# Kernel tuning notes

Measured on AMD Instinct MI355X. Metric: run time of the kernel, lower is better.

The kernel has to match this reference:

```python
import jax, jax.numpy as jnp
import numpy as np


def setup_inputs() -> dict:
    key = jax.random.key(0)
    k0, k1, k2, k3, k4 = jax.random.split(key, 5)
    B, N, H, d, kproj = 4, 2048, 8, 32, 256
    queries = jax.random.normal(k0, (B, N, H, d), dtype=jnp.float32)
    keys = jax.random.normal(k1, (B, N, H, d), dtype=jnp.float32)
    values = jax.random.normal(k2, (B, N, H, d), dtype=jnp.float32)
    # Linformer sequence projections [N, k]; scaled so projected K/V keep unit-ish variance
    E_proj = jax.random.normal(k3, (N, kproj), dtype=jnp.float32) * 0.02
    F_proj = jax.random.normal(k4, (N, kproj), dtype=jnp.float32) * 0.02
    return {"queries": queries, "keys": keys, "values": values,
            "E_proj": E_proj, "F_proj": F_proj}


def reference(queries, keys, values, E_proj, F_proj):
    """Hybrid attention of dsfa_former:
      (1) FullAttention with triangular causal mask (manual einsum+softmax)
      (2) LinearAttentionHead: Linformer-style sequence projection of K/V via E/F.
    Dropout is identity (eval). Returns (out_full, out_lin), each [B, N, H, d].
    """
    B, N, H, d = queries.shape
    scale = 1.0 / jnp.sqrt(jnp.asarray(d, queries.dtype))

    # ---- FullAttention (causal) ----
    scores = jnp.einsum('blhe,bshe->bhls', queries, keys)  # [B,H,N,N]
    causal = jnp.triu(jnp.ones((N, N), dtype=bool), k=1)   # True above diag -> masked
    scores = jnp.where(causal, -jnp.inf, scores)
    A = jax.nn.softmax(scale * scores, axis=-1)
    out_full = jnp.einsum('bhls,bshd->blhd', A, values)    # [B,N,H,d]

    # ---- LinearAttentionHead (Linformer, no causal mask since kp != N) ----
    Qb = queries.transpose(0, 2, 1, 3)  # [B,H,N,d]
    Kb = keys.transpose(0, 2, 1, 3)
    Vb = values.transpose(0, 2, 1, 3)
    Kp = jnp.einsum('bhnd,nk->bhkd', Kb, E_proj)           # [B,H,k,d]
    Vp = jnp.einsum('bhnd,nk->bhkd', Vb, F_proj)           # [B,H,k,d]
    s_lin = jnp.einsum('bhnd,bhkd->bhnk', Qb, Kp) * scale  # d_k == d
    P = jax.nn.softmax(s_lin, axis=-1)
    out_lin = jnp.einsum('bhnk,bhkd->bhnd', P, Vp).transpose(0, 2, 1, 3)  # [B,N,H,d]

    return out_full, out_lin
```

## Files before the change

### kernel.cpp

```cpp
#include <hip/hip_runtime.h>
#include <hip/hip_bf16.h>


typedef __bf16 bf16x8 __attribute__((ext_vector_type(8)));
typedef float f32x4 __attribute__((ext_vector_type(4)));

union BF8 { uint4 u4; ushort us[8]; bf16x8 b; unsigned u32[4]; };

constexpr int B_ = 4, N_ = 2048, H_ = 8, D_ = 32, KP_ = 256, BH_ = 32;
constexpr float SCALE = 0.17677669529663687f;
constexpr float SCL2 = 0.25505654442633533f;
constexpr int NFULL = 2048;

__device__ __forceinline__ ushort f2bf(float f) {
  unsigned u = __builtin_bit_cast(unsigned, f);
  return (ushort)((u + 0x7FFFu + ((u >> 16) & 1u)) >> 16);
}
__device__ __forceinline__ unsigned pk2(float f0, float f1) {
  unsigned u0 = __builtin_bit_cast(unsigned, f0) + 0x8000u;
  unsigned u1 = __builtin_bit_cast(unsigned, f1) + 0x8000u;
  return __builtin_amdgcn_perm(u1, u0, 0x07060302);
}

__device__ __forceinline__ void load8_bf(const float* __restrict__ p,
                                         float scale, BF8& hi) {
  float4 a = *reinterpret_cast<const float4*>(p);
  float4 b = *reinterpret_cast<const float4*>(p + 4);
  float x[8] = {a.x, a.y, a.z, a.w, b.x, b.y, b.z, b.w};
#pragma unroll
  for (int i = 0; i < 8; ++i) hi.us[i] = f2bf(x[i] * scale);
}

__global__ __launch_bounds__(256) void k_prep(const float* __restrict__ K,
                                              const float* __restrict__ V,
                                              const float* __restrict__ E,
                                              const float* __restrict__ F,
                                              ushort* __restrict__ KH,
                                              ushort* __restrict__ Kt,
                                              ushort* __restrict__ Vt,
                                              ushort* __restrict__ Et,
                                              ushort* __restrict__ Ft) {
  __shared__ alignas(16) ushort S[4224];
  const int idx = blockIdx.x;
  const int t = threadIdx.x;
  if (idx < 1024) {
    ushort* Tk = S;
    ushort* Tv = S + 2112;
    const int bh = idx >> 5, b = bh >> 3, h = bh & 7;
    const int n0 = (idx & 31) * 64;
    {
      const int row = t >> 2, e8 = (t & 3) * 8;
      const size_t gbase = ((size_t)(b * N_ + n0 + row) * H_ + h) * D_ + e8;
      float4 k0 = *reinterpret_cast<const float4*>(K + gbase);
      float4 k1 = *reinterpret_cast<const float4*>(K + gbase + 4);
      float4 v0 = *reinterpret_cast<const float4*>(V + gbase);
      float4 v1 = *reinterpret_cast<const float4*>(V + gbase + 4);
      float kk[8] = {k0.x,k0.y,k0.z,k0.w,k1.x,k1.y,k1.z,k1.w};
      float vv[8] = {v0.x,v0.y,v0.z,v0.w,v1.x,v1.y,v1.z,v1.w};
      BF8 xh;
#pragma unroll
      for (int i = 0; i < 8; ++i) {
        xh.us[i] = f2bf(kk[i]);
        Tk[(e8 + i) * 66 + row] = xh.us[i];
        Tv[(e8 + i) * 66 + row] = f2bf(vv[i]);
      }
      *reinterpret_cast<uint4*>(KH + ((size_t)bh * N_ + n0 + row) * D_ + e8) = xh.u4;
    }
    __syncthreads();
    {
      const int e = t >> 3, n8 = (t & 7) * 8;
      BF8 xk, xv;
#pragma unroll
      for (int i = 0; i < 8; ++i) {
        xk.us[i] = Tk[e * 66 + n8 + i];
        xv.us[i] = Tv[e * 66 + n8 + i];
      }
      const size_t ob = ((size_t)bh * D_ + e) * N_ + n0 + n8;
      *reinterpret_cast<uint4*>(Kt + ob) = xk.u4;
      *reinterpret_cast<uint4*>(Vt + ob) = xv.u4;
    }
  } else {
    const int j = idx - 1024;
    const float* src = (j >> 7) ? F : E;
    ushort* dst = (j >> 7) ? Ft : Et;
    const int jj = j & 127;
    const int n0 = (jj & 31) * 64, kp0 = (jj >> 5) * 64;
    ushort* T = S;
    {
      const int n = t >> 2, c16 = (t & 3) * 16;
      const size_t gbase = (size_t)(n0 + n) * KP_ + kp0 + c16;
#pragma unroll
      for (int q = 0; q < 4; ++q) {
        float4 x = *reinterpret_cast<const float4*>(src + gbase + q * 4);
        T[(c16 + q * 4 + 0) * 66 + n] = f2bf(x.x);
        T[(c16 + q * 4 + 1) * 66 + n] = f2bf(x.y);
        T[(c16 + q * 4 + 2) * 66 + n] = f2bf(x.z);
        T[(c16 + q * 4 + 3) * 66 + n] = f2bf(x.w);
      }
    }
    __syncthreads();
    {
      const int kp = t >> 2, n16 = (t & 3) * 16;
      BF8 x0, x1;
#pragma unroll
      for (int i = 0; i < 8; ++i) {
        x0.us[i] = T[kp * 66 + n16 + i];
        x1.us[i] = T[kp * 66 + n16 + 8 + i];
      }
      const size_t ob = (size_t)(kp0 + kp) * N_ + n0 + n16;
      *reinterpret_cast<uint4*>(dst + ob) = x0.u4;
      *reinterpret_cast<uint4*>(dst + ob + 8) = x1.u4;
    }
  }
}

__global__ __launch_bounds__(256) void k_linproj(const ushort* __restrict__ Et,
                                                 const ushort* __restrict__ Ft,
                                                 const ushort* __restrict__ Kt,
                                                 const ushort* __restrict__ Vt,
                                                 ushort* __restrict__ Kp,
                                                 ushort* __restrict__ Vpt) {
  __shared__ float L[4][64][16];
  const int bh = blockIdx.y;
  const int t = threadIdx.x;
  const int w = t >> 6, lane = t & 63, quad = lane >> 4, l15 = lane & 15;
  const int kp16 = blockIdx.x * 16;
  const int nbase = w * (N_ / 4);

  const ushort* eA = Et + (size_t)(kp16 + l15) * N_ + nbase + quad * 8;
  const ushort* fA = Ft + (size_t)(kp16 + l15) * N_ + nbase + quad * 8;
  const ushort* kB0 = Kt + ((size_t)bh * D_ + l15) * N_ + nbase + quad * 8;
  const ushort* kB1 = kB0 + (size_t)16 * N_;
  const ushort* vB0 = Vt + ((size_t)bh * D_ + l15) * N_ + nbase + quad * 8;
  const ushort* vB1 = vB0 + (size_t)16 * N_;

  f32x4 accK0 = {0.f,0.f,0.f,0.f}, accK1 = {0.f,0.f,0.f,0.f};
  f32x4 accV0 = {0.f,0.f,0.f,0.f}, accV1 = {0.f,0.f,0.f,0.f};

  for (int n0 = 0; n0 < N_ / 4; n0 += 32) {
    BF8 aE, aF, b0, b1, b2, b3;
    aE.u4 = *reinterpret_cast<const uint4*>(eA + n0);
    aF.u4 = *reinterpret_cast<const uint4*>(fA + n0);
    b0.u4 = *reinterpret_cast<const uint4*>(kB0 + n0);
    b1.u4 = *reinterpret_cast<const uint4*>(kB1 + n0);
    b2.u4 = *reinterpret_cast<const uint4*>(vB0 + n0);
    b3.u4 = *reinterpret_cast<const uint4*>(vB1 + n0);
    accK0 = __builtin_amdgcn_mfma_f32_16x16x32_bf16(aE.b, b0.b, accK0, 0, 0, 0);
    accK1 = __builtin_amdgcn_mfma_f32_16x16x32_bf16(aE.b, b1.b, accK1, 0, 0, 0);
    accV0 = __builtin_amdgcn_mfma_f32_16x16x32_bf16(aF.b, b2.b, accV0, 0, 0, 0);
    accV1 = __builtin_amdgcn_mfma_f32_16x16x32_bf16(aF.b, b3.b, accV1, 0, 0, 0);
  }

#pragma unroll
  for (int r = 0; r < 4; ++r) {
    L[w][lane][r]      = accK0[r];
    L[w][lane][4 + r]  = accK1[r];
    L[w][lane][8 + r]  = accV0[r];
    L[w][lane][12 + r] = accV1[r];
  }
  __syncthreads();
#pragma unroll
  for (int r = 0; r < 4; ++r) {
    const float v = L[0][lane][w * 4 + r] + L[1][lane][w * 4 + r] +
                    L[2][lane][w * 4 + r] + L[3][lane][w * 4 + r];
    const int kp = kp16 + quad * 4 + r;
    if (w == 0)      Kp[((size_t)bh * KP_ + kp) * D_ + l15]       = f2bf(v);
    else if (w == 1) Kp[((size_t)bh * KP_ + kp) * D_ + 16 + l15]  = f2bf(v);
    else if (w == 2) Vpt[((size_t)bh * D_ + l15) * KP_ + kp]      = f2bf(v);
    else             Vpt[((size_t)bh * D_ + 16 + l15) * KP_ + kp] = f2bf(v);
  }
}

__global__ __launch_bounds__(256) void k_attn(const float* __restrict__ Q,
                                              const ushort* __restrict__ KH,
                                              const ushort* __restrict__ Vt,
                                              const ushort* __restrict__ Kp,
                                              const ushort* __restrict__ Vpt,
                                              float* __restrict__ out) {
  __shared__ float Op[4][2][64][9];
  const int idx = blockIdx.x;
  const int t = threadIdx.x;
  const int w = t >> 6, lane = t & 63;
  const int quad = lane >> 4, l15 = lane & 15;
  const int kperm1 = 8 * (l15 >> 2) + (l15 & 3);
  const int kperm2 = kperm1 + 4;
  const f32x4 z = {0.f,0.f,0.f,0.f};

  if (idx < NFULL) {
    const int bh = (idx & 7) + 8 * ((idx >> 3) & 3);
    const int u = 63 - (idx >> 5);
    const int b = bh >> 3, h = bh & 7;
    const int q0A = 32 * u, q0B = q0A + 16;

    BF8 qhA, qhB;
    load8_bf(Q + ((size_t)(b * N_ + q0A + l15) * H_ + h) * D_ + quad * 8, SCL2, qhA);
    load8_bf(Q + ((size_t)(b * N_ + q0B + l15) * H_ + h) * D_ + quad * 8, SCL2, qhB);

    const ushort* KHb = KH + (size_t)bh * N_ * D_ + quad * 8;
    const ushort* Vt0 = Vt + ((size_t)bh * D_ + l15) * N_ + quad * 8;
    const ushort* Vt1 = Vt0 + (size_t)16 * N_;

    const int cb = (w * u) >> 2;
    const int ce = ((w + 1) * u) >> 2;

    f32x4 O0A = z, O1A = z, O0B = z, O1B = z;
    float lsumA = 0.f, lsumB = 0.f;

    BF8 k1, k2, v0, v1;
    const bool active = (cb < ce) || (w == 3);
    {
      const int c = (cb < ce) ? cb : u;
      if (active) {
        k1.u4 = *reinterpret_cast<const uint4*>(KHb + (size_t)(c * 32 + kperm1) * D_);
        k2.u4 = *reinterpret_cast<const uint4*>(KHb + (size_t)(c * 32 + kperm2) * D_);
        v0.u4 = *reinterpret_cast<const uint4*>(Vt0 + c * 32);
        v1.u4 = *reinterpret_cast<const uint4*>(Vt1 + c * 32);
      }
    }

    for (int c = cb; c < ce; ++c) {
      const int cn = (c + 1 < ce) ? c + 1 : u;
      BF8 n1, n2, n3, n4;
      n1.u4 = *reinterpret_cast<const uint4*>(KHb + (size_t)(cn * 32 + kperm1) * D_);
      n2.u4 = *reinterpret_cast<const uint4*>(KHb + (size_t)(cn * 32 + kperm2) * D_);
      n3.u4 = *reinterpret_cast<const uint4*>(Vt0 + cn * 32);
      n4.u4 = *reinterpret_cast<const uint4*>(Vt1 + cn * 32);

      f32x4 sA1 = __builtin_amdgcn_mfma_f32_16x16x32_bf16(k1.b, qhA.b, z, 0, 0, 0);
      f32x4 sA2 = __builtin_amdgcn_mfma_f32_16x16x32_bf16(k2.b, qhA.b, z, 0, 0, 0);
      f32x4 sB1 = __builtin_amdgcn_mfma_f32_16x16x32_bf16(k1.b, qhB.b, z, 0, 0, 0);
      f32x4 sB2 = __builtin_amdgcn_mfma_f32_16x16x32_bf16(k2.b, qhB.b, z, 0, 0, 0);
      float eA[8], eB[8];
#pragma unroll
      for (int r = 0; r < 4; ++r) {
        eA[r] = exp2f(sA1[r]); eA[4 + r] = exp2f(sA2[r]);
        eB[r] = exp2f(sB1[r]); eB[4 + r] = exp2f(sB2[r]);
      }
#pragma unroll
      for (int j = 0; j < 8; ++j) { lsumA += eA[j]; lsumB += eB[j]; }
      BF8 pA, pB;
      pA.u32[0] = pk2(eA[0], eA[1]); pA.u32[1] = pk2(eA[2], eA[3]);
      pA.u32[2] = pk2(eA[4], eA[5]); pA.u32[3] = pk2(eA[6], eA[7]);
      pB.u32[0] = pk2(eB[0], eB[1]); pB.u32[1] = pk2(eB[2], eB[3]);
      pB.u32[2] = pk2(eB[4], eB[5]); pB.u32[3] = pk2(eB[6], eB[7]);
      O0A = __builtin_amdgcn_mfma_f32_16x16x32_bf16(pA.b, v0.b, O0A, 0, 0, 0);
      O1A = __builtin_amdgcn_mfma_f32_16x16x32_bf16(pA.b, v1.b, O1A, 0, 0, 0);
      O0B = __builtin_amdgcn_mfma_f32_16x16x32_bf16(pB.b, v0.b, O0B, 0, 0, 0);
      O1B = __builtin_amdgcn_mfma_f32_16x16x32_bf16(pB.b, v1.b, O1B, 0, 0, 0);

      k1 = n1; k2 = n2; v0 = n3; v1 = n4;
    }

    if (w == 3) {
      f32x4 sA1 = __builtin_amdgcn_mfma_f32_16x16x32_bf16(k1.b, qhA.b, z, 0, 0, 0);
      f32x4 sA2 = __builtin_amdgcn_mfma_f32_16x16x32_bf16(k2.b, qhA.b, z, 0, 0, 0);
      f32x4 sB1 = __builtin_amdgcn_mfma_f32_16x16x32_bf16(k1.b, qhB.b, z, 0, 0, 0);
      f32x4 sB2 = __builtin_amdgcn_mfma_f32_16x16x32_bf16(k2.b, qhB.b, z, 0, 0, 0);
      float eA[8], eB[8];
#pragma unroll
      for (int j = 0; j < 8; ++j) {
        const int kk = 8 * quad + j;
        const float svA = (j < 4) ? sA1[j] : sA2[j - 4];
        const float svB = (j < 4) ? sB1[j] : sB2[j - 4];
        eA[j] = (kk <= l15)      ? exp2f(svA) : 0.f;
        eB[j] = (kk <= 16 + l15) ? exp2f(svB) : 0.f;
        lsumA += eA[j]; lsumB += eB[j];
      }
      BF8 pA, pB;
      pA.u32[0] = pk2(eA[0], eA[1]); pA.u32[1] = pk2(eA[2], eA[3]);
      pA.u32[2] = pk2(eA[4], eA[5]); pA.u32[3] = pk2(eA[6], eA[7]);
      pB.u32[0] = pk2(eB[0], eB[1]); pB.u32[1] = pk2(eB[2], eB[3]);
      pB.u32[2] = pk2(eB[4], eB[5]); pB.u32[3] = pk2(eB[6], eB[7]);
      O0A = __builtin_amdgcn_mfma_f32_16x16x32_bf16(pA.b, v0.b, O0A, 0, 0, 0);
      O1A = __builtin_amdgcn_mfma_f32_16x16x32_bf16(pA.b, v1.b, O1A, 0, 0, 0);
      O0B = __builtin_amdgcn_mfma_f32_16x16x32_bf16(pB.b, v0.b, O0B, 0, 0, 0);
      O1B = __builtin_amdgcn_mfma_f32_16x16x32_bf16(pB.b, v1.b, O1B, 0, 0, 0);
    }

#pragma unroll
    for (int r = 0; r < 4; ++r) {
      Op[w][0][lane][r] = O0A[r];  Op[w][0][lane][4 + r] = O1A[r];
      Op[w][1][lane][r] = O0B[r];  Op[w][1][lane][4 + r] = O1B[r];
    }
    Op[w][0][lane][8] = lsumA;
    Op[w][1][lane][8] = lsumB;
    __syncthreads();
    if (w < 2) {
      float l = Op[0][w][lane][8] + Op[1][w][lane][8] +
                Op[2][w][lane][8] + Op[3][w][lane][8];
      l += __shfl_xor(l, 16);
      l += __shfl_xor(l, 32);
      const float inv = 1.f / l;
      f32x4 A0, A1;
#pragma unroll
      for (int r = 0; r < 4; ++r) {
        A0[r] = Op[0][w][lane][r] + Op[1][w][lane][r] +
                Op[2][w][lane][r] + Op[3][w][lane][r];
        A1[r] = Op[0][w][lane][4+r] + Op[1][w][lane][4+r] +
                Op[2][w][lane][4+r] + Op[3][w][lane][4+r];
      }
      const int q0 = q0A + 16 * w;
#pragma unroll
      for (int r = 0; r < 4; ++r) {
        const float fr = __shfl(inv, quad * 4 + r, 16);
        const int q = q0 + quad * 4 + r;
        const size_t base = ((size_t)(b * N_ + q) * H_ + h) * D_;
        out[base + l15]      = A0[r] * fr;
        out[base + 16 + l15] = A1[r] * fr;
      }
    }
  } else {
    const int j = idx - NFULL;
    const int bh = (j & 7) + 8 * ((j >> 3) & 3);
    const int b = bh >> 3, h = bh & 7;
    const int q0 = (j >> 5) * 64 + w * 16;
    float* olin = out + (size_t)B_ * N_ * H_ * D_;

    BF8 qh;
    load8_bf(Q + ((size_t)(b * N_ + q0 + l15) * H_ + h) * D_ + quad * 8, SCL2, qh);

    const ushort* KpHb = Kp + (size_t)bh * KP_ * D_ + quad * 8;
    const ushort* Vp0 = Vpt + ((size_t)bh * D_ + l15) * KP_ + quad * 8;
    const ushort* Vp1 = Vp0 + (size_t)16 * KP_;

    f32x4 s1[8], s2[8];
    float sum = 0.f;
#pragma unroll
    for (int g = 0; g < 8; ++g) {
      const int kp0 = g * 32;
      BF8 a1, a2;
      a1.u4 = *reinterpret_cast<const uint4*>(KpHb + (size_t)(kp0 + kperm1) * D_);
      a2.u4 = *reinterpret_cast<const uint4*>(KpHb + (size_t)(kp0 + kperm2) * D_);
      s1[g] = __builtin_amdgcn_mfma_f32_16x16x32_bf16(a1.b, qh.b, z, 0, 0, 0);
      s2[g] = __builtin_amdgcn_mfma_f32_16x16x32_bf16(a2.b, qh.b, z, 0, 0, 0);
#pragma unroll
      for (int r = 0; r < 4; ++r) {
        s1[g][r] = exp2f(s1[g][r]);
        s2[g][r] = exp2f(s2[g][r]);
        sum += s1[g][r] + s2[g][r];
      }
    }
    sum += __shfl_xor(sum, 16);
    sum += __shfl_xor(sum, 32);
    const float inv = 1.f / sum;

    f32x4 O0 = z, O1 = z;
#pragma unroll
    for (int g = 0; g < 8; ++g) {
      BF8 p;
      p.u32[0] = pk2(s1[g][0] * inv, s1[g][1] * inv);
      p.u32[1] = pk2(s1[g][2] * inv, s1[g][3] * inv);
      p.u32[2] = pk2(s2[g][0] * inv, s2[g][1] * inv);
      p.u32[3] = pk2(s2[g][2] * inv, s2[g][3] * inv);
      BF8 v0, v1;
      v0.u4 = *reinterpret_cast<const uint4*>(Vp0 + g * 32);
      v1.u4 = *reinterpret_cast<const uint4*>(Vp1 + g * 32);
      O0 = __builtin_amdgcn_mfma_f32_16x16x32_bf16(p.b, v0.b, O0, 0, 0, 0);
      O1 = __builtin_amdgcn_mfma_f32_16x16x32_bf16(p.b, v1.b, O1, 0, 0, 0);
    }

#pragma unroll
    for (int r = 0; r < 4; ++r) {
      const int q = q0 + quad * 4 + r;
      const size_t base = ((size_t)(b * N_ + q) * H_ + h) * D_;
      olin[base + l15]      = O0[r];
      olin[base + 16 + l15] = O1[r];
    }
  }
}

extern "C" void kernel_launch(void* const* d_in, const int* in_sizes, int n_in,
                              void* d_out, int out_size, void* d_ws, size_t ws_size,
                              hipStream_t stream) {
  const float* Q = (const float*)d_in[0];
  const float* K = (const float*)d_in[1];
  const float* V = (const float*)d_in[2];
  const float* E = (const float*)d_in[3];
  const float* F = (const float*)d_in[4];
  float* out = (float*)d_out;

  ushort* KH  = (ushort*)d_ws;
  ushort* Kt  = KH + (size_t)BH_ * N_ * D_;
  ushort* Vt  = Kt + (size_t)BH_ * N_ * D_;
  ushort* Et  = Vt + (size_t)BH_ * N_ * D_;
  ushort* Ft  = Et + (size_t)KP_ * N_;
  ushort* Kp  = Ft + (size_t)KP_ * N_;
  ushort* Vpt = Kp + (size_t)BH_ * KP_ * D_;

  k_prep<<<dim3(1280), 256, 0, stream>>>(K, V, E, F, KH, Kt, Vt, Et, Ft);
  k_linproj<<<dim3(KP_ / 16, BH_), 256, 0, stream>>>(Et, Ft, Kt, Vt, Kp, Vpt);
  k_attn<<<dim3(NFULL + 1024), 256, 0, stream>>>(Q, KH, Vt, Kp, Vpt, out);
}
```

Measured before the change: 150.3 us.

## Enlarge causal attention tile to 64 queries per block with double-buffered K/V

Each full-attention block now covers 64 query rows (four 16-row Q fragments) instead of 32, halving the block count and reusing every loaded K/V chunk across four query tiles. K/V loads are double-buffered across two alternating register sets, and diagonal masking is split between warps 2 and 3. Partial outputs are exchanged through shared memory as packed bf16 rather than fp32, and conversions use the hardware packed bf16 convert plus the fast reciprocal. In exchange there is higher register pressure, fewer blocks for load balance, and some precision loss when the cross-warp partials are reduced in bf16.

```diff
diff --git a/kernel.cpp b/kernel.cpp
--- a/kernel.cpp
+++ b/kernel.cpp
@@ -3,23 +3,35 @@
 
 
 typedef __bf16 bf16x8 __attribute__((ext_vector_type(8)));
+typedef __bf16 bf16x2 __attribute__((ext_vector_type(2)));
 typedef float f32x4 __attribute__((ext_vector_type(4)));
 
 union BF8 { uint4 u4; ushort us[8]; bf16x8 b; unsigned u32[4]; };
 
 constexpr int B_ = 4, N_ = 2048, H_ = 8, D_ = 32, KP_ = 256, BH_ = 32;
-constexpr float SCALE = 0.17677669529663687f;
 constexpr float SCL2 = 0.25505654442633533f;
-constexpr int NFULL = 2048;
+constexpr int NFULL = 1024;
+constexpr int CHK = 32 * D_;
 
 __device__ __forceinline__ ushort f2bf(float f) {
   unsigned u = __builtin_bit_cast(unsigned, f);
   return (ushort)((u + 0x7FFFu + ((u >> 16) & 1u)) >> 16);
 }
-__device__ __forceinline__ unsigned pk2(float f0, float f1) {
+__device__ __forceinline__ unsigned pkbf(float f0, float f1) {
+#if __has_builtin(__builtin_amdgcn_cvt_pk_bf16_f32)
+  bf16x2 r = __builtin_amdgcn_cvt_pk_bf16_f32(f0, f1);
+  return __builtin_bit_cast(unsigned, r);
+#else
   unsigned u0 = __builtin_bit_cast(unsigned, f0) + 0x8000u;
   unsigned u1 = __builtin_bit_cast(unsigned, f1) + 0x8000u;
   return __builtin_amdgcn_perm(u1, u0, 0x07060302);
+#endif
+}
+__device__ __forceinline__ float bflo(unsigned u) {
+  return __builtin_bit_cast(float, u << 16);
+}
+__device__ __forceinline__ float bfhi(unsigned u) {
+  return __builtin_bit_cast(float, u & 0xFFFF0000u);
 }
 
 __device__ __forceinline__ void load8_bf(const float* __restrict__ p,
@@ -177,133 +189,169 @@
                                               const ushort* __restrict__ Kp,
                                               const ushort* __restrict__ Vpt,
                                               float* __restrict__ out) {
-  __shared__ float Op[4][2][64][9];
+  __shared__ unsigned Op[4][4][64][5];
   const int idx = blockIdx.x;
   const int t = threadIdx.x;
   const int w = t >> 6, lane = t & 63;
   const int quad = lane >> 4, l15 = lane & 15;
   const int kperm1 = 8 * (l15 >> 2) + (l15 & 3);
-  const int kperm2 = kperm1 + 4;
   const f32x4 z = {0.f,0.f,0.f,0.f};
 
   if (idx < NFULL) {
     const int bh = (idx & 7) + 8 * ((idx >> 3) & 3);
-    const int u = 63 - (idx >> 5);
+    const int m = 31 - (idx >> 5);
     const int b = bh >> 3, h = bh & 7;
-    const int q0A = 32 * u, q0B = q0A + 16;
-
-    BF8 qhA, qhB;
-    load8_bf(Q + ((size_t)(b * N_ + q0A + l15) * H_ + h) * D_ + quad * 8, SCL2, qhA);
-    load8_bf(Q + ((size_t)(b * N_ + q0B + l15) * H_ + h) * D_ + quad * 8, SCL2, qhB);
-
-    const ushort* KHb = KH + (size_t)bh * N_ * D_ + quad * 8;
-    const ushort* Vt0 = Vt + ((size_t)bh * D_ + l15) * N_ + quad * 8;
-    const ushort* Vt1 = Vt0 + (size_t)16 * N_;
-
-    const int cb = (w * u) >> 2;
-    const int ce = ((w + 1) * u) >> 2;
-
-    f32x4 O0A = z, O1A = z, O0B = z, O1B = z;
-    float lsumA = 0.f, lsumB = 0.f;
-
-    BF8 k1, k2, v0, v1;
-    const bool active = (cb < ce) || (w == 3);
+    const int q0 = 64 * m;
+
+    BF8 qh[4];
+#pragma unroll
+    for (int tt = 0; tt < 4; ++tt)
+      load8_bf(Q + ((size_t)(b * N_ + q0 + 16 * tt + l15) * H_ + h) * D_ + quad * 8,
+               SCL2, qh[tt]);
+
+    const ushort* KHl = KH + (size_t)bh * N_ * D_ + (size_t)kperm1 * D_ + quad * 8;
+    const ushort* V0l = Vt + ((size_t)bh * D_ + l15) * N_ + quad * 8;
+    const ushort* V1l = V0l + (size_t)16 * N_;
+
+    const int nun = 2 * m;
+    const int cb = (w * nun) >> 2;
+    const int ce = ((w + 1) * nun) >> 2;
+    const int nwu = ce - cb;
+
+    f32x4 O0[4], O1[4];
+    float ls[4];
+#pragma unroll
+    for (int tt = 0; tt < 4; ++tt) { O0[tt] = z; O1[tt] = z; ls[tt] = 0.f; }
+
+    BF8 kA1, kA2, vA0, vA1, kB1, kB2, vB0, vB1;
+
+    auto procU = [&](BF8& k1, BF8& k2, BF8& v0, BF8& v1) {
+#pragma unroll
+      for (int tt = 0; tt < 4; ++tt) {
+        f32x4 s1 = __builtin_amdgcn_mfma_f32_16x16x32_bf16(k1.b, qh[tt].b, z, 0, 0, 0);
+        f32x4 s2 = __builtin_amdgcn_mfma_f32_16x16x32_bf16(k2.b, qh[tt].b, z, 0, 0, 0);
+        float e0 = exp2f(s1[0]), e1 = exp2f(s1[1]), e2 = exp2f(s1[2]), e3 = exp2f(s1[3]);
+        float e4 = exp2f(s2[0]), e5 = exp2f(s2[1]), e6 = exp2f(s2[2]), e7 = exp2f(s2[3]);
+        ls[tt] += ((e0 + e1) + (e2 + e3)) + ((e4 + e5) + (e6 + e7));
+        BF8 p;
+        p.u32[0] = pkbf(e0, e1); p.u32[1] = pkbf(e2, e3);
+        p.u32[2] = pkbf(e4, e5); p.u32[3] = pkbf(e6, e7);
+        O0[tt] = __builtin_amdgcn_mfma_f32_16x16x32_bf16(p.b, v0.b, O0[tt], 0, 0, 0);
+        O1[tt] = __builtin_amdgcn_mfma_f32_16x16x32_bf16(p.b, v1.b, O1[tt], 0, 0, 0);
+      }
+    };
+    auto procM = [&](BF8& k1, BF8& k2, BF8& v0, BF8& v1, int ta, bool doUnm) {
+#pragma unroll
+      for (int d = 0; d < 2; ++d) {
+        const int tt = ta + d;
+        const int thr = d ? 16 + l15 : l15;
+        f32x4 s1 = __builtin_amdgcn_mfma_f32_16x16x32_bf16(k1.b, qh[tt].b, z, 0, 0, 0);
+        f32x4 s2 = __builtin_amdgcn_mfma_f32_16x16x32_bf16(k2.b, qh[tt].b, z, 0, 0, 0);
+        float e[8];
+#pragma unroll
+        for (int j = 0; j < 8; ++j) {
+          const float sv = (j < 4) ? s1[j] : s2[j - 4];
+          e[j] = (8 * quad + j <= thr) ? exp2f(sv) : 0.f;
+        }
+        ls[tt] += ((e[0] + e[1]) + (e[2] + e[3])) + ((e[4] + e[5]) + (e[6] + e[7]));
+        BF8 p;
+        p.u32[0] = pkbf(e[0], e[1]); p.u32[1] = pkbf(e[2], e[3]);
+        p.u32[2] = pkbf(e[4], e[5]); p.u32[3] = pkbf(e[6], e[7]);
+        O0[tt] = __builtin_amdgcn_mfma_f32_16x16x32_bf16(p.b, v0.b, O0[tt], 0, 0, 0);
+        O1[tt] = __builtin_amdgcn_mfma_f32_16x16x32_bf16(p.b, v1.b, O1[tt], 0, 0, 0);
+      }
+      if (doUnm) {
+#pragma unroll
+        for (int tt = 2; tt < 4; ++tt) {
+          f32x4 s1 = __builtin_amdgcn_mfma_f32_16x16x32_bf16(k1.b, qh[tt].b, z, 0, 0, 0);
+          f32x4 s2 = __builtin_amdgcn_mfma_f32_16x16x32_bf16(k2.b, qh[tt].b, z, 0, 0, 0);
+          float e0 = exp2f(s1[0]), e1 = exp2f(s1[1]), e2 = exp2f(s1[2]), e3 = exp2f(s1[3]);
+          float e4 = exp2f(s2[0]), e5 = exp2f(s2[1]), e6 = exp2f(s2[2]), e7 = exp2f(s2[3]);
+          ls[tt] += ((e0 + e1) + (e2 + e3)) + ((e4 + e5) + (e6 + e7));
+          BF8 p;
+          p.u32[0] = pkbf(e0, e1); p.u32[1] = pkbf(e2, e3);
+          p.u32[2] = pkbf(e4, e5); p.u32[3] = pkbf(e6, e7);
+          O0[tt] = __builtin_amdgcn_mfma_f32_16x16x32_bf16(p.b, v0.b, O0[tt], 0, 0, 0);
+          O1[tt] = __builtin_amdgcn_mfma_f32_16x16x32_bf16(p.b, v1.b, O1[tt], 0, 0, 0);
+        }
+      }
+    };
+
+    kA1.u4 = *reinterpret_cast<const uint4*>(KHl + (size_t)cb * CHK);
+    kA2.u4 = *reinterpret_cast<const uint4*>(KHl + (size_t)cb * CHK + 4 * D_);
+    vA0.u4 = *reinterpret_cast<const uint4*>(V0l + cb * 32);
+    vA1.u4 = *reinterpret_cast<const uint4*>(V1l + cb * 32);
+    kB1.u4 = *reinterpret_cast<const uint4*>(KHl + (size_t)(cb + 1) * CHK);
+    kB2.u4 = *reinterpret_cast<const uint4*>(KHl + (size_t)(cb + 1) * CHK + 4 * D_);
+    vB0.u4 = *reinterpret_cast<const uint4*>(V0l + (cb + 1) * 32);
+    vB1.u4 = *reinterpret_cast<const uint4*>(V1l + (cb + 1) * 32);
+
+    const ushort* pKA = KHl + (size_t)(cb + 2) * CHK;
+    const ushort* pKB = KHl + (size_t)(cb + 3) * CHK;
+    const ushort* pV0 = V0l + (cb + 2) * 32;
+    const ushort* pV1 = V1l + (cb + 2) * 32;
+
+    int i = 0;
+    for (; i + 2 <= nwu; i += 2) {
+      procU(kA1, kA2, vA0, vA1);
+      kA1.u4 = *reinterpret_cast<const uint4*>(pKA);
+      kA2.u4 = *reinterpret_cast<const uint4*>(pKA + 4 * D_);
+      vA0.u4 = *reinterpret_cast<const uint4*>(pV0);
+      vA1.u4 = *reinterpret_cast<const uint4*>(pV1);
+      procU(kB1, kB2, vB0, vB1);
+      kB1.u4 = *reinterpret_cast<const uint4*>(pKB);
+      kB2.u4 = *reinterpret_cast<const uint4*>(pKB + 4 * D_);
+      vB0.u4 = *reinterpret_cast<const uint4*>(pV0 + 32);
+      vB1.u4 = *reinterpret_cast<const uint4*>(pV1 + 32);
+      pKA += 2 * CHK; pKB += 2 * CHK; pV0 += 64; pV1 += 64;
+    }
+    if (i < nwu) {
+      procU(kA1, kA2, vA0, vA1);
+      if (w == 3) procM(kB1, kB2, vB0, vB1, 0, true);
+    } else if (w == 3) {
+      procM(kA1, kA2, vA0, vA1, 0, true);
+    }
+    if (w == 2) {
+      const int c2 = nun + 1;
+      kB1.u4 = *reinterpret_cast<const uint4*>(KHl + (size_t)c2 * CHK);
+      kB2.u4 = *reinterpret_cast<const uint4*>(KHl + (size_t)c2 * CHK + 4 * D_);
+      vB0.u4 = *reinterpret_cast<const uint4*>(V0l + c2 * 32);
+      vB1.u4 = *reinterpret_cast<const uint4*>(V1l + c2 * 32);
+      procM(kB1, kB2, vB0, vB1, 2, false);
+    }
+
+#pragma unroll
+    for (int tt = 0; tt < 4; ++tt) {
+      Op[w][tt][lane][0] = pkbf(O0[tt][0], O0[tt][1]);
+      Op[w][tt][lane][1] = pkbf(O0[tt][2], O0[tt][3]);
+      Op[w][tt][lane][2] = pkbf(O1[tt][0], O1[tt][1]);
+      Op[w][tt][lane][3] = pkbf(O1[tt][2], O1[tt][3]);
+      Op[w][tt][lane][4] = __builtin_bit_cast(unsigned, ls[tt]);
+    }
+    __syncthreads();
     {
-      const int c = (cb < ce) ? cb : u;
-      if (active) {
-        k1.u4 = *reinterpret_cast<const uint4*>(KHb + (size_t)(c * 32 + kperm1) * D_);
-        k2.u4 = *reinterpret_cast<const uint4*>(KHb + (size_t)(c * 32 + kperm2) * D_);
-        v0.u4 = *reinterpret_cast<const uint4*>(Vt0 + c * 32);
-        v1.u4 = *reinterpret_cast<const uint4*>(Vt1 + c * 32);
-      }
-    }
-
-    for (int c = cb; c < ce; ++c) {
-      const int cn = (c + 1 < ce) ? c + 1 : u;
-      BF8 n1, n2, n3, n4;
-      n1.u4 = *reinterpret_cast<const uint4*>(KHb + (size_t)(cn * 32 + kperm1) * D_);
-      n2.u4 = *reinterpret_cast<const uint4*>(KHb + (size_t)(cn * 32 + kperm2) * D_);
-      n3.u4 = *reinterpret_cast<const uint4*>(Vt0 + cn * 32);
-      n4.u4 = *reinterpret_cast<const uint4*>(Vt1 + cn * 32);
-
-      f32x4 sA1 = __builtin_amdgcn_mfma_f32_16x16x32_bf16(k1.b, qhA.b, z, 0, 0, 0);
-      f32x4 sA2 = __builtin_amdgcn_mfma_f32_16x16x32_bf16(k2.b, qhA.b, z, 0, 0, 0);
-      f32x4 sB1 = __builtin_amdgcn_mfma_f32_16x16x32_bf16(k1.b, qhB.b, z, 0, 0, 0);
-      f32x4 sB2 = __builtin_amdgcn_mfma_f32_16x16x32_bf16(k2.b, qhB.b, z, 0, 0, 0);
-      float eA[8], eB[8];
-#pragma unroll
-      for (int r = 0; r < 4; ++r) {
-        eA[r] = exp2f(sA1[r]); eA[4 + r] = exp2f(sA2[r]);
-        eB[r] = exp2f(sB1[r]); eB[4 + r] = exp2f(sB2[r]);
-      }
-#pragma unroll
-      for (int j = 0; j < 8; ++j) { lsumA += eA[j]; lsumB += eB[j]; }
-      BF8 pA, pB;
-      pA.u32[0] = pk2(eA[0], eA[1]); pA.u32[1] = pk2(eA[2], eA[3]);
-      pA.u32[2] = pk2(eA[4], eA[5]); pA.u32[3] = pk2(eA[6], eA[7]);
-      pB.u32[0] = pk2(eB[0], eB[1]); pB.u32[1] = pk2(eB[2], eB[3]);
-      pB.u32[2] = pk2(eB[4], eB[5]); pB.u32[3] = pk2(eB[6], eB[7]);
-      O0A = __builtin_amdgcn_mfma_f32_16x16x32_bf16(pA.b, v0.b, O0A, 0, 0, 0);
-      O1A = __builtin_amdgcn_mfma_f32_16x16x32_bf16(pA.b, v1.b, O1A, 0, 0, 0);
-      O0B = __builtin_amdgcn_mfma_f32_16x16x32_bf16(pB.b, v0.b, O0B, 0, 0, 0);
-      O1B = __builtin_amdgcn_mfma_f32_16x16x32_bf16(pB.b, v1.b, O1B, 0, 0, 0);
-
-      k1 = n1; k2 = n2; v0 = n3; v1 = n4;
-    }
-
-    if (w == 3) {
-      f32x4 sA1 = __builtin_amdgcn_mfma_f32_16x16x32_bf16(k1.b, qhA.b, z, 0, 0, 0);
-      f32x4 sA2 = __builtin_amdgcn_mfma_f32_16x16x32_bf16(k2.b, qhA.b, z, 0, 0, 0);
-      f32x4 sB1 = __builtin_amdgcn_mfma_f32_16x16x32_bf16(k1.b, qhB.b, z, 0, 0, 0);
-      f32x4 sB2 = __builtin_amdgcn_mfma_f32_16x16x32_bf16(k2.b, qhB.b, z, 0, 0, 0);
-      float eA[8], eB[8];
-#pragma unroll
-      for (int j = 0; j < 8; ++j) {
-        const int kk = 8 * quad + j;
-        const float svA = (j < 4) ? sA1[j] : sA2[j - 4];
-        const float svB = (j < 4) ? sB1[j] : sB2[j - 4];
-        eA[j] = (kk <= l15)      ? exp2f(svA) : 0.f;
-        eB[j] = (kk <= 16 + l15) ? exp2f(svB) : 0.f;
-        lsumA += eA[j]; lsumB += eB[j];
-      }
-      BF8 pA, pB;
-      pA.u32[0] = pk2(eA[0], eA[1]); pA.u32[1] = pk2(eA[2], eA[3]);
-      pA.u32[2] = pk2(eA[4], eA[5]); pA.u32[3] = pk2(eA[6], eA[7]);
-      pB.u32[0] = pk2(eB[0], eB[1]); pB.u32[1] = pk2(eB[2], eB[3]);
-      pB.u32[2] = pk2(eB[4], eB[5]); pB.u32[3] = pk2(eB[6], eB[7]);
-      O0A = __builtin_amdgcn_mfma_f32_16x16x32_bf16(pA.b, v0.b, O0A, 0, 0, 0);
-      O1A = __builtin_amdgcn_mfma_f32_16x16x32_bf16(pA.b, v1.b, O1A, 0, 0, 0);
-      O0B = __builtin_amdgcn_mfma_f32_16x16x32_bf16(pB.b, v0.b, O0B, 0, 0, 0);
-      O1B = __builtin_amdgcn_mfma_f32_16x16x32_bf16(pB.b, v1.b, O1B, 0, 0, 0);
-    }
-
-#pragma unroll
-    for (int r = 0; r < 4; ++r) {
-      Op[w][0][lane][r] = O0A[r];  Op[w][0][lane][4 + r] = O1A[r];
-      Op[w][1][lane][r] = O0B[r];  Op[w][1][lane][4 + r] = O1B[r];
-    }
-    Op[w][0][lane][8] = lsumA;
-    Op[w][1][lane][8] = lsumB;
-    __syncthreads();
-    if (w < 2) {
-      float l = Op[0][w][lane][8] + Op[1][w][lane][8] +
-                Op[2][w][lane][8] + Op[3][w][lane][8];
+      const int tt = w;
+      float l = __builtin_bit_cast(float, Op[0][tt][lane][4]) +
+                __builtin_bit_cast(float, Op[1][tt][lane][4]) +
+                __builtin_bit_cast(float, Op[2][tt][lane][4]) +
+                __builtin_bit_cast(float, Op[3][tt][lane][4]);
       l += __shfl_xor(l, 16);
       l += __shfl_xor(l, 32);
-      const float inv = 1.f / l;
-      f32x4 A0, A1;
-#pragma unroll
-      for (int r = 0; r < 4; ++r) {
-        A0[r] = Op[0][w][lane][r] + Op[1][w][lane][r] +
-                Op[2][w][lane][r] + Op[3][w][lane][r];
-        A1[r] = Op[0][w][lane][4+r] + Op[1][w][lane][4+r] +
-                Op[2][w][lane][4+r] + Op[3][w][lane][4+r];
-      }
-      const int q0 = q0A + 16 * w;
+      const float inv = __builtin_amdgcn_rcpf(l);
+      float A0[4] = {0.f,0.f,0.f,0.f}, A1[4] = {0.f,0.f,0.f,0.f};
+#pragma unroll
+      for (int s = 0; s < 4; ++s) {
+        const unsigned u0 = Op[s][tt][lane][0], u1 = Op[s][tt][lane][1];
+        const unsigned u2 = Op[s][tt][lane][2], u3 = Op[s][tt][lane][3];
+        A0[0] += bflo(u0); A0[1] += bfhi(u0);
+        A0[2] += bflo(u1); A0[3] += bfhi(u1);
+        A1[0] += bflo(u2); A1[1] += bfhi(u2);
+        A1[2] += bflo(u3); A1[3] += bfhi(u3);
+      }
 #pragma unroll
       for (int r = 0; r < 4; ++r) {
         const float fr = __shfl(inv, quad * 4 + r, 16);
-        const int q = q0 + quad * 4 + r;
+        const int q = q0 + 16 * tt + quad * 4 + r;
         const size_t base = ((size_t)(b * N_ + q) * H_ + h) * D_;
         out[base + l15]      = A0[r] * fr;
         out[base + 16 + l15] = A1[r] * fr;
@@ -319,6 +367,7 @@
     BF8 qh;
     load8_bf(Q + ((size_t)(b * N_ + q0 + l15) * H_ + h) * D_ + quad * 8, SCL2, qh);
 
+    const int kperm2 = kperm1 + 4;
     const ushort* KpHb = Kp + (size_t)bh * KP_ * D_ + quad * 8;
     const ushort* Vp0 = Vpt + ((size_t)bh * D_ + l15) * KP_ + quad * 8;
     const ushort* Vp1 = Vp0 + (size_t)16 * KP_;
@@ -342,16 +391,16 @@
     }
     sum += __shfl_xor(sum, 16);
     sum += __shfl_xor(sum, 32);
-    const float inv = 1.f / sum;
+    const float inv = __builtin_amdgcn_rcpf(sum);
 
     f32x4 O0 = z, O1 = z;
 #pragma unroll
     for (int g = 0; g < 8; ++g) {
       BF8 p;
-      p.u32[0] = pk2(s1[g][0] * inv, s1[g][1] * inv);
-      p.u32[1] = pk2(s1[g][2] * inv, s1[g][3] * inv);
-      p.u32[2] = pk2(s2[g][0] * inv, s2[g][1] * inv);
-      p.u32[3] = pk2(s2[g][2] * inv, s2[g][3] * inv);
+      p.u32[0] = pkbf(s1[g][0] * inv, s1[g][1] * inv);
+      p.u32[1] = pkbf(s1[g][2] * inv, s1[g][3] * inv);
+      p.u32[2] = pkbf(s2[g][0] * inv, s2[g][1] * inv);
+      p.u32[3] = pkbf(s2[g][2] * inv, s2[g][3] * inv);
       BF8 v0, v1;
       v0.u4 = *reinterpret_cast<const uint4*>(Vp0 + g * 32);
       v1.u4 = *reinterpret_cast<const uint4*>(Vp1 + g * 32);
```

Result: faster. 145.9 us (-2.9%).
